# Performance work log

Hardware: AMD Instinct MI355X
Metric: run time of the kernel (lower is better)

Reference implementation:

```python
import jax, jax.numpy as jnp
import numpy as np

T, H, E, K, I, SHARED = 2048, 1024, 64, 6, 512, 2
SI = I * SHARED  # shared-expert intermediate size


def setup_inputs() -> dict:
    key = jax.random.key(0)
    ks = jax.random.split(key, 10)
    s = 0.02
    return {
        "hidden_states": jax.random.normal(ks[0], (T, H), jnp.float32),
        "gate_w": jax.random.normal(ks[1], (E, H), jnp.float32) * s,
        "gate_bias": jax.random.normal(ks[2], (1, E), jnp.float32) * s,
        "w_gate": jax.random.normal(ks[3], (E, H, I), jnp.float32) * s,
        "w_up": jax.random.normal(ks[4], (E, H, I), jnp.float32) * s,
        "w_down": jax.random.normal(ks[5], (E, I, H), jnp.float32) * s,
        "ws_gate": jax.random.normal(ks[6], (H, SI), jnp.float32) * s,
        "ws_up": jax.random.normal(ks[7], (H, SI), jnp.float32) * s,
        "ws_down": jax.random.normal(ks[8], (SI, H), jnp.float32) * s,
    }


def reference(hidden_states, gate_w, gate_bias, w_gate, w_up, w_down, ws_gate, ws_up, ws_down):
    x = hidden_states  # [T, H]
    # shared expert (Ernie4MLP, SwiGLU)
    shared = (jax.nn.silu(x @ ws_gate) * (x @ ws_up)) @ ws_down  # [T, H]
    # router gate
    logits = x @ gate_w.T                      # [T, E]
    scores = jax.nn.sigmoid(logits)            # [T, E]
    # top-k selection on bias-corrected scores, weights from uncorrected scores
    _, idx = jax.lax.top_k(scores + gate_bias, K)          # [T, K]
    w = jnp.take_along_axis(scores, idx, axis=1)           # [T, K]
    w = w / jnp.sum(w, axis=1, keepdims=True)              # renormalize
    # combine weights per (token, expert)
    cmb = jnp.zeros((T, E), x.dtype).at[jnp.arange(T)[:, None], idx].add(w)  # [T, E]
    # grouped expert SwiGLU FFN (dense reference over all experts)
    g = jnp.einsum("th,ehi->tei", x, w_gate)   # [T, E, I]
    u = jnp.einsum("th,ehi->tei", x, w_up)     # [T, E, I]
    a = jax.nn.silu(g) * u * cmb[:, :, None]   # weight before down-proj
    moe_out = jnp.einsum("tei,eih->th", a, w_down)  # [T, H]
    return moe_out + shared
```

## Files before the change

### kernel.cpp

```cpp
#include <hip/hip_runtime.h>

#define T_TOK 2048
#define H_DIM 1024
#define E_NUM 64
#define TOPK  6
#define I_DIM 512
#define SI_DIM 1024
#define CAP   320

typedef __attribute__((ext_vector_type(8))) short bf16x8;
typedef __attribute__((ext_vector_type(4))) float f32x4;
typedef __attribute__((ext_vector_type(4))) short short4v;

#define BSTR 36

__device__ __forceinline__ short f2bf(float f) {
  union { float f; unsigned u; } v; v.f = f;
  unsigned r = v.u + 0x7FFFu + ((v.u >> 16) & 1u);
  return (short)(r >> 16);
}
__device__ __forceinline__ float bf2f(short s) {
  union { unsigned u; float f; } v;
  v.u = ((unsigned)(unsigned short)s) << 16;
  return v.f;
}
__device__ __forceinline__ unsigned pack2(float lo, float hi) {
  return ((unsigned)(unsigned short)f2bf(hi) << 16) | (unsigned)(unsigned short)f2bf(lo);
}

__device__ __forceinline__ void gl_lds16(const short* g, short* l) {
  __builtin_amdgcn_global_load_lds(
      (const __attribute__((address_space(1))) unsigned int*)g,
      (__attribute__((address_space(3))) unsigned int*)l, 16, 0, 0);
}

__global__ __launch_bounds__(256) void cvt_kernel(const float* __restrict__ x,
                                                  short* __restrict__ xb) {
  int i = (blockIdx.x * 256 + threadIdx.x) * 4;
  float4 v = *(const float4*)(x + i);
  short4v o;
  o[0] = f2bf(v.x); o[1] = f2bf(v.y); o[2] = f2bf(v.z); o[3] = f2bf(v.w);
  *(short4v*)(xb + i) = o;
}

__global__ void zero_kernel(int* __restrict__ cnt) {
  if (threadIdx.x < E_NUM + 1) cnt[threadIdx.x] = 0;
}

__global__ __launch_bounds__(256) void router_kernel(const float* __restrict__ x,
                                                     const float* __restrict__ gw,
                                                     float* __restrict__ scores) {
  int t = blockIdx.x * 4 + (threadIdx.x >> 6);
  int e = threadIdx.x & 63;
  const float4* xr = (const float4*)(x + (size_t)t * H_DIM);
  const float4* wr = (const float4*)(gw + (size_t)e * H_DIM);
  float s = 0.f;
  #pragma unroll 4
  for (int i = 0; i < H_DIM / 4; i++) {
    float4 a = xr[i], b = wr[i];
    s = fmaf(a.x, b.x, s); s = fmaf(a.y, b.y, s);
    s = fmaf(a.z, b.z, s); s = fmaf(a.w, b.w, s);
  }
  scores[t * E_NUM + e] = 1.f / (1.f + __expf(-s));
}

__global__ __launch_bounds__(64) void topk_kernel(const float* __restrict__ scores,
                                                  const float* __restrict__ bias,
                                                  int* __restrict__ cnt,
                                                  float* __restrict__ wts,
                                                  int* __restrict__ qmap,
                                                  unsigned* __restrict__ pairs,
                                                  int* __restrict__ dslot) {
  int t = blockIdx.x;
  int e = threadIdx.x;
  float s = scores[t * E_NUM + e];
  float c = s + bias[e];
  int selected = 0;
  float sum = 0.f;
  for (int k = 0; k < TOPK; k++) {
    float v = c; int idx = e;
    #pragma unroll
    for (int off = 32; off > 0; off >>= 1) {
      float v2 = __shfl_xor(v, off);
      int  i2 = __shfl_xor(idx, off);
      if (v2 > v || (v2 == v && i2 < idx)) { v = v2; idx = i2; }
    }
    sum += __shfl(s, idx);
    if (e == idx) { selected = 1; c = -__builtin_inff(); }
  }
  unsigned long long m = __ballot(selected);
  if (selected) {
    int rank = __popcll(m & ((1ull << e) - 1ull));
    int pos = atomicAdd(&cnt[e], 1);
    int qid = atomicAdd(&cnt[E_NUM], 1);
    if (pos >= CAP) pos = CAP - 1;
    int slot = e * CAP + pos;
    wts[slot] = s / sum;
    qmap[slot] = qid;
    pairs[qid] = ((unsigned)t << 16) | (unsigned)slot;
    dslot[t * TOPK + rank] = qid;
  }
}

__global__ __launch_bounds__(128) void gather_kernel(const unsigned* __restrict__ pairs,
                                                     const short* __restrict__ xb,
                                                     short* __restrict__ Xg) {
  unsigned pr = pairs[blockIdx.x];
  int t = pr >> 16, slot = pr & 0xFFFF;
  int i = threadIdx.x * 8;
  *(bf16x8*)(Xg + (size_t)slot * H_DIM + i) =
      *(const bf16x8*)(xb + (size_t)t * H_DIM + i);
}


__global__ __launch_bounds__(512) void gemm_up_all(
    const short* __restrict__ xb,
    const float* __restrict__ wsg, const float* __restrict__ wsu,
    short* __restrict__ Gs, short* __restrict__ Us,
    const short* __restrict__ Xg,
    const float* __restrict__ wg, const float* __restrict__ wu,
    short* __restrict__ Gm, short* __restrict__ Um,
    const int* __restrict__ cnt)
{
  __shared__ short As[256 * 32], Bs[128 * BSTR];
  const int bid = blockIdx.x;
  const short* A; const float* Bf; short* O;
  int m0, n0, count, N;
  const int K = H_DIM;
  if (bid < 128) {
    const int m = bid >> 4, nidx = bid & 15;
    m0 = m * 256; n0 = (nidx & 7) * 128;
    A = xb; Bf = (nidx < 8) ? wsg : wsu; O = (nidx < 8) ? Gs : Us;
    count = T_TOK; N = SI_DIM;
  } else {
    const int b = bid - 128;
    const int e = b & 63, rest = b >> 6;
    const int mm = rest & 1, z = rest >> 1;
    count = cnt[e]; if (count > CAP) count = CAP;
    m0 = mm * 256;
    if (m0 >= count) return;
    n0 = (z & 3) * 128;
    A = Xg + (size_t)e * CAP * H_DIM;
    Bf = ((z < 4) ? wg : wu) + (size_t)e * (size_t)I_DIM * H_DIM;
    O = ((z < 4) ? Gm : Um) + (size_t)e * (size_t)CAP * I_DIM;
    N = I_DIM;
  }
  const int lane = threadIdx.x & 63, wave = threadIdx.x >> 6;
  const int quad = lane >> 4, l16 = lane & 15;
  const int wm = wave >> 1, wn = wave & 1;
  const int srow = lane >> 2, schk = lane & 3;
  const int bn4 = (threadIdx.x & 31) * 4;
  const int bkp = (threadIdx.x >> 5) * 2;

  f32x4 acc[4][4];
  #pragma unroll
  for (int i = 0; i < 4; i++)
    #pragma unroll
    for (int j = 0; j < 4; j++) acc[i][j] = (f32x4){0.f, 0.f, 0.f, 0.f};

  for (int ko = 0; ko < K; ko += 32) {
    __syncthreads();
    float4 b0 = *(const float4*)(Bf + (size_t)(ko + bkp) * N + n0 + bn4);
    float4 b1 = *(const float4*)(Bf + (size_t)(ko + bkp + 1) * N + n0 + bn4);
    {
      const int rb0 = wave * 32;
      gl_lds16(A + (size_t)(m0 + rb0 + srow) * K + ko + schk * 8, &As[rb0 * 32]);
      gl_lds16(A + (size_t)(m0 + rb0 + 16 + srow) * K + ko + schk * 8, &As[(rb0 + 16) * 32]);
    }
    *(unsigned*)&Bs[(bn4 + 0) * BSTR + bkp] = pack2(b0.x, b1.x);
    *(unsigned*)&Bs[(bn4 + 1) * BSTR + bkp] = pack2(b0.y, b1.y);
    *(unsigned*)&Bs[(bn4 + 2) * BSTR + bkp] = pack2(b0.z, b1.z);
    *(unsigned*)&Bs[(bn4 + 3) * BSTR + bkp] = pack2(b0.w, b1.w);
    __syncthreads();
    bf16x8 a[4], b[4];
    #pragma unroll
    for (int mt = 0; mt < 4; mt++)
      a[mt] = *(const bf16x8*)&As[(wm * 64 + mt * 16 + l16) * 32 + quad * 8];
    #pragma unroll
    for (int nt = 0; nt < 4; nt++) {
      const int row = wn * 64 + nt * 16 + l16;
      short4v lo = *(const short4v*)&Bs[row * BSTR + quad * 8];
      short4v hi = *(const short4v*)&Bs[row * BSTR + quad * 8 + 4];
      #pragma unroll
      for (int j = 0; j < 4; j++) { b[nt][j] = lo[j]; b[nt][j + 4] = hi[j]; }
    }
    #pragma unroll
    for (int mt = 0; mt < 4; mt++)
      #pragma unroll
      for (int nt = 0; nt < 4; nt++)
        acc[mt][nt] = __builtin_amdgcn_mfma_f32_16x16x32_bf16(a[mt], b[nt], acc[mt][nt], 0, 0, 0);
  }

  #pragma unroll
  for (int mt = 0; mt < 4; mt++) {
    #pragma unroll
    for (int reg = 0; reg < 4; reg++) {
      int gr = m0 + wm * 64 + mt * 16 + quad * 4 + reg;
      if (gr >= count) continue;
      size_t ro = (size_t)gr * N;
      #pragma unroll
      for (int nt = 0; nt < 4; nt++)
        O[ro + n0 + wn * 64 + nt * 16 + l16] = f2bf(acc[mt][nt][reg]);
    }
  }
}

__global__ __launch_bounds__(256) void swiglu_all(
    const unsigned* __restrict__ pairs, const float* __restrict__ wts,
    short* __restrict__ Gs, const short* __restrict__ Us,
    const short* __restrict__ Gm, const short* __restrict__ Um,
    short* __restrict__ Hbuf) {
  const int bid = blockIdx.x;
  if (bid < T_TOK * SI_DIM / 2048) {
    size_t i = ((size_t)bid * 256 + threadIdx.x) * 8;
    bf16x8 g8 = *(const bf16x8*)(Gs + i);
    bf16x8 u8 = *(const bf16x8*)(Us + i);
    bf16x8 o;
    #pragma unroll
    for (int j = 0; j < 8; j++) {
      float g = bf2f(g8[j]), u = bf2f(u8[j]);
      o[j] = f2bf((g / (1.f + __expf(-g))) * u);
    }
    *(bf16x8*)(Gs + i) = o;
  } else {
    int qid = (bid - T_TOK * SI_DIM / 2048) * 4 + (threadIdx.x >> 6);
    unsigned pr = pairs[qid];
    int slot = pr & 0xFFFF;
    float wt = wts[slot];
    int i = (threadIdx.x & 63) * 8;
    bf16x8 g8 = *(const bf16x8*)(Gm + (size_t)slot * I_DIM + i);
    bf16x8 u8 = *(const bf16x8*)(Um + (size_t)slot * I_DIM + i);
    bf16x8 o;
    #pragma unroll
    for (int j = 0; j < 8; j++) {
      float g = bf2f(g8[j]), u = bf2f(u8[j]);
      o[j] = f2bf((g / (1.f + __expf(-g))) * u * wt);
    }
    *(bf16x8*)(Hbuf + (size_t)slot * I_DIM + i) = o;
  }
}

__global__ __launch_bounds__(512) void gemm_down_all(
    const short* __restrict__ Hs, const float* __restrict__ wsd,
    float* __restrict__ out,
    const short* __restrict__ Hbuf, const float* __restrict__ wd,
    float* __restrict__ Pbuf, const int* __restrict__ qmap,
    const int* __restrict__ cnt)
{
  __shared__ short As[256 * 32], Bs[128 * BSTR];
  const int bid = blockIdx.x;
  const short* A; const float* Bf; float* OutP;
  const int* qm = nullptr;
  int m0, n0, count, K;
  const int N = H_DIM;
  if (bid < 64) {
    const int m = bid >> 3, n = bid & 7;
    m0 = m * 256; n0 = n * 128;
    A = Hs; Bf = wsd; OutP = out;
    count = T_TOK; K = SI_DIM;
  } else {
    const int b = bid - 64;
    const int e = b & 63, rest = b >> 6;
    const int mm = rest & 1, z = rest >> 1;
    count = cnt[e]; if (count > CAP) count = CAP;
    m0 = mm * 256;
    if (m0 >= count) return;
    n0 = z * 128;
    A = Hbuf + (size_t)e * (size_t)CAP * I_DIM;
    Bf = wd + (size_t)e * (size_t)I_DIM * H_DIM;
    OutP = Pbuf;
    qm = qmap + e * CAP;
    K = I_DIM;
  }
  const int lane = threadIdx.x & 63, wave = threadIdx.x >> 6;
  const int quad = lane >> 4, l16 = lane & 15;
  const int wm = wave >> 1, wn = wave & 1;
  const int srow = lane >> 2, schk = lane & 3;
  const int bn4 = (threadIdx.x & 31) * 4;
  const int bkp = (threadIdx.x >> 5) * 2;

  f32x4 acc[4][4];
  #pragma unroll
  for (int i = 0; i < 4; i++)
    #pragma unroll
    for (int j = 0; j < 4; j++) acc[i][j] = (f32x4){0.f, 0.f, 0.f, 0.f};

  for (int ko = 0; ko < K; ko += 32) {
    __syncthreads();
    float4 b0 = *(const float4*)(Bf + (size_t)(ko + bkp) * N + n0 + bn4);
    float4 b1 = *(const float4*)(Bf + (size_t)(ko + bkp + 1) * N + n0 + bn4);
    {
      const int rb0 = wave * 32;
      gl_lds16(A + (size_t)(m0 + rb0 + srow) * K + ko + schk * 8, &As[rb0 * 32]);
      gl_lds16(A + (size_t)(m0 + rb0 + 16 + srow) * K + ko + schk * 8, &As[(rb0 + 16) * 32]);
    }
    *(unsigned*)&Bs[(bn4 + 0) * BSTR + bkp] = pack2(b0.x, b1.x);
    *(unsigned*)&Bs[(bn4 + 1) * BSTR + bkp] = pack2(b0.y, b1.y);
    *(unsigned*)&Bs[(bn4 + 2) * BSTR + bkp] = pack2(b0.z, b1.z);
    *(unsigned*)&Bs[(bn4 + 3) * BSTR + bkp] = pack2(b0.w, b1.w);
    __syncthreads();
    bf16x8 a[4], b[4];
    #pragma unroll
    for (int mt = 0; mt < 4; mt++)
      a[mt] = *(const bf16x8*)&As[(wm * 64 + mt * 16 + l16) * 32 + quad * 8];
    #pragma unroll
    for (int nt = 0; nt < 4; nt++) {
      const int row = wn * 64 + nt * 16 + l16;
      short4v lo = *(const short4v*)&Bs[row * BSTR + quad * 8];
      short4v hi = *(const short4v*)&Bs[row * BSTR + quad * 8 + 4];
      #pragma unroll
      for (int j = 0; j < 4; j++) { b[nt][j] = lo[j]; b[nt][j + 4] = hi[j]; }
    }
    #pragma unroll
    for (int mt = 0; mt < 4; mt++)
      #pragma unroll
      for (int nt = 0; nt < 4; nt++)
        acc[mt][nt] = __builtin_amdgcn_mfma_f32_16x16x32_bf16(a[mt], b[nt], acc[mt][nt], 0, 0, 0);
  }

  #pragma unroll
  for (int mt = 0; mt < 4; mt++) {
    #pragma unroll
    for (int reg = 0; reg < 4; reg++) {
      int gr = m0 + wm * 64 + mt * 16 + quad * 4 + reg;
      if (gr >= count) continue;
      size_t ro = qm ? (size_t)qm[gr] * H_DIM : (size_t)gr * H_DIM;
      #pragma unroll
      for (int nt = 0; nt < 4; nt++)
        OutP[ro + n0 + wn * 64 + nt * 16 + l16] = acc[mt][nt][reg];
    }
  }
}

__global__ __launch_bounds__(256) void combine_kernel(float* __restrict__ out,
                                                      const float* __restrict__ Pbuf,
                                                      const int* __restrict__ dslot) {
  int t = blockIdx.x;
  int c = threadIdx.x * 4;
  float4 acc = *(float4*)(out + (size_t)t * H_DIM + c);
  #pragma unroll
  for (int k = 0; k < TOPK; k++) {
    int q = dslot[t * TOPK + k];
    float4 p = *(const float4*)(Pbuf + (size_t)q * H_DIM + c);
    acc.x += p.x; acc.y += p.y; acc.z += p.z; acc.w += p.w;
  }
  *(float4*)(out + (size_t)t * H_DIM + c) = acc;
}

extern "C" void kernel_launch(void* const* d_in, const int* in_sizes, int n_in,
                              void* d_out, int out_size, void* d_ws, size_t ws_size,
                              hipStream_t stream) {
  (void)in_sizes; (void)n_in; (void)out_size; (void)ws_size;
  const float* x       = (const float*)d_in[0];
  const float* gate_w  = (const float*)d_in[1];
  const float* gate_b  = (const float*)d_in[2];
  const float* w_gate  = (const float*)d_in[3];
  const float* w_up    = (const float*)d_in[4];
  const float* w_down  = (const float*)d_in[5];
  const float* ws_gate = (const float*)d_in[6];
  const float* ws_up   = (const float*)d_in[7];
  const float* ws_down = (const float*)d_in[8];
  float* out = (float*)d_out;

  char* base = (char*)d_ws;
  size_t off = 0;
  auto alloc = [&](size_t bytes) {
    char* r = base + off; off += (bytes + 255) & ~(size_t)255; return r;
  };
  float*    scores = (float*)   alloc((size_t)T_TOK * E_NUM * 4);
  int*      cnt    = (int*)     alloc(72 * 4);
  unsigned* pairs  = (unsigned*)alloc((size_t)T_TOK * TOPK * 4);
  float*    wts    = (float*)   alloc((size_t)E_NUM * CAP * 4);
  int*      qmap   = (int*)     alloc((size_t)E_NUM * CAP * 4);
  int*      dslot  = (int*)     alloc((size_t)T_TOK * TOPK * 4);
  short*    xb     = (short*)   alloc((size_t)T_TOK * H_DIM * 2);
  char*     reg1   = alloc((size_t)E_NUM * CAP * H_DIM * 2);
  float*    Pbuf   = (float*)   alloc((size_t)T_TOK * TOPK * H_DIM * 4);
  short*    Gm     = (short*)   alloc((size_t)E_NUM * CAP * I_DIM * 2);
  short*    Um     = (short*)   alloc((size_t)E_NUM * CAP * I_DIM * 2);
  short*    Gs     = (short*)   alloc((size_t)T_TOK * SI_DIM * 2);
  short*    Us     = (short*)   alloc((size_t)T_TOK * SI_DIM * 2);

  short* Xg   = (short*)reg1;
  short* Hbuf = (short*)reg1;
  short* Hs   = Gs;

  cvt_kernel<<<T_TOK * H_DIM / 1024, 256, 0, stream>>>(x, xb);
  zero_kernel<<<1, 128, 0, stream>>>(cnt);
  router_kernel<<<T_TOK / 4, 256, 0, stream>>>(x, gate_w, scores);
  topk_kernel<<<T_TOK, 64, 0, stream>>>(scores, gate_b, cnt, wts, qmap, pairs, dslot);
  gather_kernel<<<T_TOK * TOPK, 128, 0, stream>>>(pairs, xb, Xg);

  gemm_up_all<<<128 + E_NUM * 16, 512, 0, stream>>>(
      xb, ws_gate, ws_up, Gs, Us, Xg, w_gate, w_up, Gm, Um, cnt);

  swiglu_all<<<T_TOK * SI_DIM / 2048 + T_TOK * TOPK / 4, 256, 0, stream>>>(
      pairs, wts, Gs, Us, Gm, Um, Hbuf);

  gemm_down_all<<<64 + E_NUM * 16, 512, 0, stream>>>(
      Hs, ws_down, out, Hbuf, w_down, Pbuf, qmap, cnt);

  combine_kernel<<<T_TOK, 256, 0, stream>>>(out, Pbuf, dslot);
}
```

Before: 607.9 us.

## Fuse gather and SwiGLU into up-projection GEMM with gate/up computed per block

The up-projection kernel now computes both the gate and up GEMMs for the same output tile in one block, keeping the gate result packed as bf16 in registers and applying SiLU, the multiply and the routing weight in the epilogue. This removes the separate swiglu kernel and the Gs/Us/Gm/Um round trips through global memory. The token gather kernel is dropped: expert A rows are loaded straight from xb through pairs/qmap indirection. The zero kernel is folded into the convert kernel. In exchange, each block runs twice as long with half as many blocks, adds register pressure from the stash, and the indirect A loads may coalesce less well.

```diff
diff --git a/kernel.cpp b/kernel.cpp
--- a/kernel.cpp
+++ b/kernel.cpp
@@ -35,16 +35,14 @@
 }
 
 __global__ __launch_bounds__(256) void cvt_kernel(const float* __restrict__ x,
-                                                  short* __restrict__ xb) {
+                                                  short* __restrict__ xb,
+                                                  int* __restrict__ cnt) {
+  if (blockIdx.x == 0 && threadIdx.x <= E_NUM) cnt[threadIdx.x] = 0;
   int i = (blockIdx.x * 256 + threadIdx.x) * 4;
   float4 v = *(const float4*)(x + i);
   short4v o;
   o[0] = f2bf(v.x); o[1] = f2bf(v.y); o[2] = f2bf(v.z); o[3] = f2bf(v.w);
   *(short4v*)(xb + i) = o;
-}
-
-__global__ void zero_kernel(int* __restrict__ cnt) {
-  if (threadIdx.x < E_NUM + 1) cnt[threadIdx.x] = 0;
 }
 
 __global__ __launch_bounds__(256) void router_kernel(const float* __restrict__ x,
@@ -102,48 +100,37 @@
   }
 }
 
-__global__ __launch_bounds__(128) void gather_kernel(const unsigned* __restrict__ pairs,
-                                                     const short* __restrict__ xb,
-                                                     short* __restrict__ Xg) {
-  unsigned pr = pairs[blockIdx.x];
-  int t = pr >> 16, slot = pr & 0xFFFF;
-  int i = threadIdx.x * 8;
-  *(bf16x8*)(Xg + (size_t)slot * H_DIM + i) =
-      *(const bf16x8*)(xb + (size_t)t * H_DIM + i);
-}
-
-
 __global__ __launch_bounds__(512) void gemm_up_all(
     const short* __restrict__ xb,
     const float* __restrict__ wsg, const float* __restrict__ wsu,
-    short* __restrict__ Gs, short* __restrict__ Us,
-    const short* __restrict__ Xg,
+    short* __restrict__ Hs,
     const float* __restrict__ wg, const float* __restrict__ wu,
-    short* __restrict__ Gm, short* __restrict__ Um,
-    const int* __restrict__ cnt)
+    short* __restrict__ Hbuf,
+    const unsigned* __restrict__ pairs, const int* __restrict__ qmap,
+    const float* __restrict__ wts, const int* __restrict__ cnt)
 {
   __shared__ short As[256 * 32], Bs[128 * BSTR];
   const int bid = blockIdx.x;
-  const short* A; const float* Bf; short* O;
-  int m0, n0, count, N;
+  const float *B0f, *B1f; short* O;
+  int m0, n0, count, N, moe, e = 0;
   const int K = H_DIM;
-  if (bid < 128) {
-    const int m = bid >> 4, nidx = bid & 15;
-    m0 = m * 256; n0 = (nidx & 7) * 128;
-    A = xb; Bf = (nidx < 8) ? wsg : wsu; O = (nidx < 8) ? Gs : Us;
-    count = T_TOK; N = SI_DIM;
+  if (bid < 64) {
+    m0 = (bid >> 3) * 256; n0 = (bid & 7) * 128;
+    B0f = wsg; B1f = wsu; O = Hs;
+    count = T_TOK; N = SI_DIM; moe = 0;
   } else {
-    const int b = bid - 128;
-    const int e = b & 63, rest = b >> 6;
-    const int mm = rest & 1, z = rest >> 1;
+    const int b = bid - 64;
+    e = b & 63;
+    const int rest = b >> 6;
+    const int mm = rest & 1, j = rest >> 1;
     count = cnt[e]; if (count > CAP) count = CAP;
     m0 = mm * 256;
     if (m0 >= count) return;
-    n0 = (z & 3) * 128;
-    A = Xg + (size_t)e * CAP * H_DIM;
-    Bf = ((z < 4) ? wg : wu) + (size_t)e * (size_t)I_DIM * H_DIM;
-    O = ((z < 4) ? Gm : Um) + (size_t)e * (size_t)CAP * I_DIM;
-    N = I_DIM;
+    n0 = j * 128;
+    B0f = wg + (size_t)e * I_DIM * H_DIM;
+    B1f = wu + (size_t)e * I_DIM * H_DIM;
+    O = Hbuf + (size_t)e * CAP * I_DIM;
+    N = I_DIM; moe = 1;
   }
   const int lane = threadIdx.x & 63, wave = threadIdx.x >> 6;
   const int quad = lane >> 4, l16 = lane & 15;
@@ -152,44 +139,64 @@
   const int bn4 = (threadIdx.x & 31) * 4;
   const int bkp = (threadIdx.x >> 5) * 2;
 
+  const int r1 = wave * 32 + srow, r2 = r1 + 16;
+  int t1 = m0 + r1, t2 = m0 + r2;
+  if (moe) {
+    t1 = (m0 + r1 < count) ? (int)(pairs[qmap[e * CAP + m0 + r1]] >> 16) : 0;
+    t2 = (m0 + r2 < count) ? (int)(pairs[qmap[e * CAP + m0 + r2]] >> 16) : 0;
+  }
+  const short* Arow1 = xb + (size_t)t1 * H_DIM + schk * 8;
+  const short* Arow2 = xb + (size_t)t2 * H_DIM + schk * 8;
+
   f32x4 acc[4][4];
   #pragma unroll
   for (int i = 0; i < 4; i++)
     #pragma unroll
-    for (int j = 0; j < 4; j++) acc[i][j] = (f32x4){0.f, 0.f, 0.f, 0.f};
-
-  for (int ko = 0; ko < K; ko += 32) {
-    __syncthreads();
-    float4 b0 = *(const float4*)(Bf + (size_t)(ko + bkp) * N + n0 + bn4);
-    float4 b1 = *(const float4*)(Bf + (size_t)(ko + bkp + 1) * N + n0 + bn4);
-    {
-      const int rb0 = wave * 32;
-      gl_lds16(A + (size_t)(m0 + rb0 + srow) * K + ko + schk * 8, &As[rb0 * 32]);
-      gl_lds16(A + (size_t)(m0 + rb0 + 16 + srow) * K + ko + schk * 8, &As[(rb0 + 16) * 32]);
-    }
-    *(unsigned*)&Bs[(bn4 + 0) * BSTR + bkp] = pack2(b0.x, b1.x);
-    *(unsigned*)&Bs[(bn4 + 1) * BSTR + bkp] = pack2(b0.y, b1.y);
-    *(unsigned*)&Bs[(bn4 + 2) * BSTR + bkp] = pack2(b0.z, b1.z);
-    *(unsigned*)&Bs[(bn4 + 3) * BSTR + bkp] = pack2(b0.w, b1.w);
-    __syncthreads();
-    bf16x8 a[4], b[4];
-    #pragma unroll
-    for (int mt = 0; mt < 4; mt++)
-      a[mt] = *(const bf16x8*)&As[(wm * 64 + mt * 16 + l16) * 32 + quad * 8];
+    for (int j2 = 0; j2 < 4; j2++) acc[i][j2] = (f32x4){0.f, 0.f, 0.f, 0.f};
+
+  auto kloop = [&](const float* Bf) {
+    for (int ko = 0; ko < K; ko += 32) {
+      __syncthreads();
+      float4 b0 = *(const float4*)(Bf + (size_t)(ko + bkp) * N + n0 + bn4);
+      float4 b1 = *(const float4*)(Bf + (size_t)(ko + bkp + 1) * N + n0 + bn4);
+      gl_lds16(Arow1 + ko, &As[(wave * 32) * 32]);
+      gl_lds16(Arow2 + ko, &As[(wave * 32 + 16) * 32]);
+      *(unsigned*)&Bs[(bn4 + 0) * BSTR + bkp] = pack2(b0.x, b1.x);
+      *(unsigned*)&Bs[(bn4 + 1) * BSTR + bkp] = pack2(b0.y, b1.y);
+      *(unsigned*)&Bs[(bn4 + 2) * BSTR + bkp] = pack2(b0.z, b1.z);
+      *(unsigned*)&Bs[(bn4 + 3) * BSTR + bkp] = pack2(b0.w, b1.w);
+      __syncthreads();
+      bf16x8 a[4], b[4];
+      #pragma unroll
+      for (int mt = 0; mt < 4; mt++)
+        a[mt] = *(const bf16x8*)&As[(wm * 64 + mt * 16 + l16) * 32 + quad * 8];
+      #pragma unroll
+      for (int nt = 0; nt < 4; nt++) {
+        const int row = wn * 64 + nt * 16 + l16;
+        short4v lo = *(const short4v*)&Bs[row * BSTR + quad * 8];
+        short4v hi = *(const short4v*)&Bs[row * BSTR + quad * 8 + 4];
+        #pragma unroll
+        for (int jj = 0; jj < 4; jj++) { b[nt][jj] = lo[jj]; b[nt][jj + 4] = hi[jj]; }
+      }
+      #pragma unroll
+      for (int mt = 0; mt < 4; mt++)
+        #pragma unroll
+        for (int nt = 0; nt < 4; nt++)
+          acc[mt][nt] = __builtin_amdgcn_mfma_f32_16x16x32_bf16(a[mt], b[nt], acc[mt][nt], 0, 0, 0);
+    }
+  };
+
+  kloop(B0f);
+  unsigned stash[4][4][2];
+  #pragma unroll
+  for (int mt = 0; mt < 4; mt++)
     #pragma unroll
     for (int nt = 0; nt < 4; nt++) {
-      const int row = wn * 64 + nt * 16 + l16;
-      short4v lo = *(const short4v*)&Bs[row * BSTR + quad * 8];
-      short4v hi = *(const short4v*)&Bs[row * BSTR + quad * 8 + 4];
-      #pragma unroll
-      for (int j = 0; j < 4; j++) { b[nt][j] = lo[j]; b[nt][j + 4] = hi[j]; }
-    }
-    #pragma unroll
-    for (int mt = 0; mt < 4; mt++)
-      #pragma unroll
-      for (int nt = 0; nt < 4; nt++)
-        acc[mt][nt] = __builtin_amdgcn_mfma_f32_16x16x32_bf16(a[mt], b[nt], acc[mt][nt], 0, 0, 0);
-  }
+      stash[mt][nt][0] = pack2(acc[mt][nt][0], acc[mt][nt][1]);
+      stash[mt][nt][1] = pack2(acc[mt][nt][2], acc[mt][nt][3]);
+      acc[mt][nt] = (f32x4){0.f, 0.f, 0.f, 0.f};
+    }
+  kloop(B1f);
 
   #pragma unroll
   for (int mt = 0; mt < 4; mt++) {
@@ -197,46 +204,16 @@
     for (int reg = 0; reg < 4; reg++) {
       int gr = m0 + wm * 64 + mt * 16 + quad * 4 + reg;
       if (gr >= count) continue;
+      float wt = moe ? wts[e * CAP + gr] : 1.f;
       size_t ro = (size_t)gr * N;
       #pragma unroll
-      for (int nt = 0; nt < 4; nt++)
-        O[ro + n0 + wn * 64 + nt * 16 + l16] = f2bf(acc[mt][nt][reg]);
-    }
-  }
-}
-
-__global__ __launch_bounds__(256) void swiglu_all(
-    const unsigned* __restrict__ pairs, const float* __restrict__ wts,
-    short* __restrict__ Gs, const short* __restrict__ Us,
-    const short* __restrict__ Gm, const short* __restrict__ Um,
-    short* __restrict__ Hbuf) {
-  const int bid = blockIdx.x;
-  if (bid < T_TOK * SI_DIM / 2048) {
-    size_t i = ((size_t)bid * 256 + threadIdx.x) * 8;
-    bf16x8 g8 = *(const bf16x8*)(Gs + i);
-    bf16x8 u8 = *(const bf16x8*)(Us + i);
-    bf16x8 o;
-    #pragma unroll
-    for (int j = 0; j < 8; j++) {
-      float g = bf2f(g8[j]), u = bf2f(u8[j]);
-      o[j] = f2bf((g / (1.f + __expf(-g))) * u);
-    }
-    *(bf16x8*)(Gs + i) = o;
-  } else {
-    int qid = (bid - T_TOK * SI_DIM / 2048) * 4 + (threadIdx.x >> 6);
-    unsigned pr = pairs[qid];
-    int slot = pr & 0xFFFF;
-    float wt = wts[slot];
-    int i = (threadIdx.x & 63) * 8;
-    bf16x8 g8 = *(const bf16x8*)(Gm + (size_t)slot * I_DIM + i);
-    bf16x8 u8 = *(const bf16x8*)(Um + (size_t)slot * I_DIM + i);
-    bf16x8 o;
-    #pragma unroll
-    for (int j = 0; j < 8; j++) {
-      float g = bf2f(g8[j]), u = bf2f(u8[j]);
-      o[j] = f2bf((g / (1.f + __expf(-g))) * u * wt);
-    }
-    *(bf16x8*)(Hbuf + (size_t)slot * I_DIM + i) = o;
+      for (int nt = 0; nt < 4; nt++) {
+        float g = bf2f((short)(stash[mt][nt][reg >> 1] >> ((reg & 1) * 16)));
+        float u = acc[mt][nt][reg];
+        O[ro + n0 + wn * 64 + nt * 16 + l16] =
+            f2bf((g / (1.f + __expf(-g))) * u * wt);
+      }
+    }
   }
 }
 
@@ -374,28 +351,16 @@
   int*      qmap   = (int*)     alloc((size_t)E_NUM * CAP * 4);
   int*      dslot  = (int*)     alloc((size_t)T_TOK * TOPK * 4);
   short*    xb     = (short*)   alloc((size_t)T_TOK * H_DIM * 2);
-  char*     reg1   = alloc((size_t)E_NUM * CAP * H_DIM * 2);
+  short*    Hbuf   = (short*)   alloc((size_t)E_NUM * CAP * I_DIM * 2);
   float*    Pbuf   = (float*)   alloc((size_t)T_TOK * TOPK * H_DIM * 4);
-  short*    Gm     = (short*)   alloc((size_t)E_NUM * CAP * I_DIM * 2);
-  short*    Um     = (short*)   alloc((size_t)E_NUM * CAP * I_DIM * 2);
-  short*    Gs     = (short*)   alloc((size_t)T_TOK * SI_DIM * 2);
-  short*    Us     = (short*)   alloc((size_t)T_TOK * SI_DIM * 2);
-
-  short* Xg   = (short*)reg1;
-  short* Hbuf = (short*)reg1;
-  short* Hs   = Gs;
-
-  cvt_kernel<<<T_TOK * H_DIM / 1024, 256, 0, stream>>>(x, xb);
-  zero_kernel<<<1, 128, 0, stream>>>(cnt);
+  short*    Hs     = (short*)   alloc((size_t)T_TOK * SI_DIM * 2);
+
+  cvt_kernel<<<T_TOK * H_DIM / 1024, 256, 0, stream>>>(x, xb, cnt);
   router_kernel<<<T_TOK / 4, 256, 0, stream>>>(x, gate_w, scores);
   topk_kernel<<<T_TOK, 64, 0, stream>>>(scores, gate_b, cnt, wts, qmap, pairs, dslot);
-  gather_kernel<<<T_TOK * TOPK, 128, 0, stream>>>(pairs, xb, Xg);
-
-  gemm_up_all<<<128 + E_NUM * 16, 512, 0, stream>>>(
-      xb, ws_gate, ws_up, Gs, Us, Xg, w_gate, w_up, Gm, Um, cnt);
-
-  swiglu_all<<<T_TOK * SI_DIM / 2048 + T_TOK * TOPK / 4, 256, 0, stream>>>(
-      pairs, wts, Gs, Us, Gm, Um, Hbuf);
+
+  gemm_up_all<<<64 + E_NUM * 8, 512, 0, stream>>>(
+      xb, ws_gate, ws_up, Hs, w_gate, w_up, Hbuf, pairs, qmap, wts, cnt);
 
   gemm_down_all<<<64 + E_NUM * 16, 512, 0, stream>>>(
       Hs, ws_down, out, Hbuf, w_down, Pbuf, qmap, cnt);
```

New measurement: 667.3 us. 9.8% more time.

## Fuse token gather into up-projection GEMM and merge cvt/zero/router kernels

Applied to the files above, without the earlier changes.

The separate gather kernel, which copied routed token rows into a per-expert buffer, is removed. The up-projection GEMM now looks up each row's token index through qmap and pairs and loads directly from the bf16 activations. The convert, counter-zeroing and router kernels are merged into one launch split by block index. This removes one intermediate write and read of the gathered activations plus two launches, at the cost of indirect, non-contiguous row loads in the GEMM.

```diff
diff --git a/kernel.cpp b/kernel.cpp
--- a/kernel.cpp
+++ b/kernel.cpp
@@ -34,34 +34,31 @@
       (__attribute__((address_space(3))) unsigned int*)l, 16, 0, 0);
 }
 
-__global__ __launch_bounds__(256) void cvt_kernel(const float* __restrict__ x,
-                                                  short* __restrict__ xb) {
-  int i = (blockIdx.x * 256 + threadIdx.x) * 4;
-  float4 v = *(const float4*)(x + i);
-  short4v o;
-  o[0] = f2bf(v.x); o[1] = f2bf(v.y); o[2] = f2bf(v.z); o[3] = f2bf(v.w);
-  *(short4v*)(xb + i) = o;
-}
-
-__global__ void zero_kernel(int* __restrict__ cnt) {
-  if (threadIdx.x < E_NUM + 1) cnt[threadIdx.x] = 0;
-}
-
-__global__ __launch_bounds__(256) void router_kernel(const float* __restrict__ x,
-                                                     const float* __restrict__ gw,
-                                                     float* __restrict__ scores) {
-  int t = blockIdx.x * 4 + (threadIdx.x >> 6);
-  int e = threadIdx.x & 63;
-  const float4* xr = (const float4*)(x + (size_t)t * H_DIM);
-  const float4* wr = (const float4*)(gw + (size_t)e * H_DIM);
-  float s = 0.f;
-  #pragma unroll 4
-  for (int i = 0; i < H_DIM / 4; i++) {
-    float4 a = xr[i], b = wr[i];
-    s = fmaf(a.x, b.x, s); s = fmaf(a.y, b.y, s);
-    s = fmaf(a.z, b.z, s); s = fmaf(a.w, b.w, s);
-  }
-  scores[t * E_NUM + e] = 1.f / (1.f + __expf(-s));
+__global__ __launch_bounds__(256) void cvt_router_kernel(
+    const float* __restrict__ x, short* __restrict__ xb, int* __restrict__ cnt,
+    const float* __restrict__ gw, float* __restrict__ scores) {
+  const int bid = blockIdx.x;
+  if (bid < T_TOK * H_DIM / 1024) {
+    if (bid == 0 && threadIdx.x <= E_NUM) cnt[threadIdx.x] = 0;
+    int i = (bid * 256 + threadIdx.x) * 4;
+    float4 v = *(const float4*)(x + i);
+    short4v o;
+    o[0] = f2bf(v.x); o[1] = f2bf(v.y); o[2] = f2bf(v.z); o[3] = f2bf(v.w);
+    *(short4v*)(xb + i) = o;
+  } else {
+    int t = (bid - T_TOK * H_DIM / 1024) * 4 + (threadIdx.x >> 6);
+    int e = threadIdx.x & 63;
+    const float4* xr = (const float4*)(x + (size_t)t * H_DIM);
+    const float4* wr = (const float4*)(gw + (size_t)e * H_DIM);
+    float s = 0.f;
+    #pragma unroll 4
+    for (int i = 0; i < H_DIM / 4; i++) {
+      float4 a = xr[i], b = wr[i];
+      s = fmaf(a.x, b.x, s); s = fmaf(a.y, b.y, s);
+      s = fmaf(a.z, b.z, s); s = fmaf(a.w, b.w, s);
+    }
+    scores[t * E_NUM + e] = 1.f / (1.f + __expf(-s));
+  }
 }
 
 __global__ __launch_bounds__(64) void topk_kernel(const float* __restrict__ scores,
@@ -102,48 +99,37 @@
   }
 }
 
-__global__ __launch_bounds__(128) void gather_kernel(const unsigned* __restrict__ pairs,
-                                                     const short* __restrict__ xb,
-                                                     short* __restrict__ Xg) {
-  unsigned pr = pairs[blockIdx.x];
-  int t = pr >> 16, slot = pr & 0xFFFF;
-  int i = threadIdx.x * 8;
-  *(bf16x8*)(Xg + (size_t)slot * H_DIM + i) =
-      *(const bf16x8*)(xb + (size_t)t * H_DIM + i);
-}
-
-
 __global__ __launch_bounds__(512) void gemm_up_all(
     const short* __restrict__ xb,
     const float* __restrict__ wsg, const float* __restrict__ wsu,
     short* __restrict__ Gs, short* __restrict__ Us,
-    const short* __restrict__ Xg,
     const float* __restrict__ wg, const float* __restrict__ wu,
     short* __restrict__ Gm, short* __restrict__ Um,
+    const unsigned* __restrict__ pairs, const int* __restrict__ qmap,
     const int* __restrict__ cnt)
 {
   __shared__ short As[256 * 32], Bs[128 * BSTR];
   const int bid = blockIdx.x;
-  const short* A; const float* Bf; short* O;
-  int m0, n0, count, N;
+  const float* Bf; short* O;
+  int m0, n0, count, N, moe = 0, e = 0;
   const int K = H_DIM;
   if (bid < 128) {
     const int m = bid >> 4, nidx = bid & 15;
     m0 = m * 256; n0 = (nidx & 7) * 128;
-    A = xb; Bf = (nidx < 8) ? wsg : wsu; O = (nidx < 8) ? Gs : Us;
+    Bf = (nidx < 8) ? wsg : wsu; O = (nidx < 8) ? Gs : Us;
     count = T_TOK; N = SI_DIM;
   } else {
     const int b = bid - 128;
-    const int e = b & 63, rest = b >> 6;
+    e = b & 63;
+    const int rest = b >> 6;
     const int mm = rest & 1, z = rest >> 1;
     count = cnt[e]; if (count > CAP) count = CAP;
     m0 = mm * 256;
     if (m0 >= count) return;
     n0 = (z & 3) * 128;
-    A = Xg + (size_t)e * CAP * H_DIM;
-    Bf = ((z < 4) ? wg : wu) + (size_t)e * (size_t)I_DIM * H_DIM;
-    O = ((z < 4) ? Gm : Um) + (size_t)e * (size_t)CAP * I_DIM;
-    N = I_DIM;
+    Bf = ((z < 4) ? wg : wu) + (size_t)e * I_DIM * H_DIM;
+    O = ((z < 4) ? Gm : Um) + (size_t)e * CAP * I_DIM;
+    N = I_DIM; moe = 1;
   }
   const int lane = threadIdx.x & 63, wave = threadIdx.x >> 6;
   const int quad = lane >> 4, l16 = lane & 15;
@@ -152,6 +138,15 @@
   const int bn4 = (threadIdx.x & 31) * 4;
   const int bkp = (threadIdx.x >> 5) * 2;
 
+  const int r1 = wave * 32 + srow, r2 = r1 + 16;
+  int t1 = m0 + r1, t2 = m0 + r2;
+  if (moe) {
+    t1 = (m0 + r1 < count) ? (int)(pairs[qmap[e * CAP + m0 + r1]] >> 16) : 0;
+    t2 = (m0 + r2 < count) ? (int)(pairs[qmap[e * CAP + m0 + r2]] >> 16) : 0;
+  }
+  const short* Arow1 = xb + (size_t)t1 * H_DIM + schk * 8;
+  const short* Arow2 = xb + (size_t)t2 * H_DIM + schk * 8;
+
   f32x4 acc[4][4];
   #pragma unroll
   for (int i = 0; i < 4; i++)
@@ -162,11 +157,8 @@
     __syncthreads();
     float4 b0 = *(const float4*)(Bf + (size_t)(ko + bkp) * N + n0 + bn4);
     float4 b1 = *(const float4*)(Bf + (size_t)(ko + bkp + 1) * N + n0 + bn4);
-    {
-      const int rb0 = wave * 32;
-      gl_lds16(A + (size_t)(m0 + rb0 + srow) * K + ko + schk * 8, &As[rb0 * 32]);
-      gl_lds16(A + (size_t)(m0 + rb0 + 16 + srow) * K + ko + schk * 8, &As[(rb0 + 16) * 32]);
-    }
+    gl_lds16(Arow1 + ko, &As[(wave * 32) * 32]);
+    gl_lds16(Arow2 + ko, &As[(wave * 32 + 16) * 32]);
     *(unsigned*)&Bs[(bn4 + 0) * BSTR + bkp] = pack2(b0.x, b1.x);
     *(unsigned*)&Bs[(bn4 + 1) * BSTR + bkp] = pack2(b0.y, b1.y);
     *(unsigned*)&Bs[(bn4 + 2) * BSTR + bkp] = pack2(b0.z, b1.z);
@@ -374,25 +366,20 @@
   int*      qmap   = (int*)     alloc((size_t)E_NUM * CAP * 4);
   int*      dslot  = (int*)     alloc((size_t)T_TOK * TOPK * 4);
   short*    xb     = (short*)   alloc((size_t)T_TOK * H_DIM * 2);
-  char*     reg1   = alloc((size_t)E_NUM * CAP * H_DIM * 2);
+  short*    Hbuf   = (short*)   alloc((size_t)E_NUM * CAP * I_DIM * 2);
   float*    Pbuf   = (float*)   alloc((size_t)T_TOK * TOPK * H_DIM * 4);
   short*    Gm     = (short*)   alloc((size_t)E_NUM * CAP * I_DIM * 2);
   short*    Um     = (short*)   alloc((size_t)E_NUM * CAP * I_DIM * 2);
   short*    Gs     = (short*)   alloc((size_t)T_TOK * SI_DIM * 2);
   short*    Us     = (short*)   alloc((size_t)T_TOK * SI_DIM * 2);
-
-  short* Xg   = (short*)reg1;
-  short* Hbuf = (short*)reg1;
-  short* Hs   = Gs;
-
-  cvt_kernel<<<T_TOK * H_DIM / 1024, 256, 0, stream>>>(x, xb);
-  zero_kernel<<<1, 128, 0, stream>>>(cnt);
-  router_kernel<<<T_TOK / 4, 256, 0, stream>>>(x, gate_w, scores);
+  short*    Hs     = Gs;
+
+  cvt_router_kernel<<<T_TOK * H_DIM / 1024 + T_TOK / 4, 256, 0, stream>>>(
+      x, xb, cnt, gate_w, scores);
   topk_kernel<<<T_TOK, 64, 0, stream>>>(scores, gate_b, cnt, wts, qmap, pairs, dslot);
-  gather_kernel<<<T_TOK * TOPK, 128, 0, stream>>>(pairs, xb, Xg);
 
   gemm_up_all<<<128 + E_NUM * 16, 512, 0, stream>>>(
-      xb, ws_gate, ws_up, Gs, Us, Xg, w_gate, w_up, Gm, Um, cnt);
+      xb, ws_gate, ws_up, Gs, Us, w_gate, w_up, Gm, Um, pairs, qmap, cnt);
 
   swiglu_all<<<T_TOK * SI_DIM / 2048 + T_TOK * TOPK / 4, 256, 0, stream>>>(
       pairs, wts, Gs, Us, Gm, Um, Hbuf);
```

Result: slower. 794.8 us (+30.7%).
